# Kernel optimization log

Measured on AMD Instinct MI355X. Metric: run time of the kernel, lower is better.

Reference implementation:

```python
import jax, jax.numpy as jnp
import numpy as np

EPS = 1.0
POS_WEIGHT = 1.0
REDUCTION = 'mean'

N, D = 8192, 128
NUM_CLASSES = 32


def setup_inputs() -> dict:
    key = jax.random.key(0)
    k1, k2 = jax.random.split(key)
    ys = jax.random.normal(k1, (N, D), dtype=jnp.float32)
    labels = jax.random.randint(k2, (N,), 0, NUM_CLASSES, dtype=jnp.int64)
    return {"ys": ys, "labels": labels}


def reference(ys, labels):
    n = ys.shape[0]
    # Pairwise squared distances via one GEMM: ||a||^2 + ||b||^2 - 2 a.b
    sq = jnp.sum(ys * ys, axis=-1)                      # [N]
    d2 = sq[:, None] + sq[None, :] - 2.0 * (ys @ ys.T)  # [N, N]
    d2 = jnp.maximum(d2, 0.0)
    pair = jnp.triu(jnp.ones((n, n), dtype=bool), k=1)  # i < j, each unordered pair once
    same = labels[:, None] == labels[None, :]
    # positive-pair term: pos_weight * squared distance
    pos = POS_WEIGHT * d2
    # negative-pair term: clip(eps - sqrt(d2), 0)^2 ; guard sqrt(0) for unused entries
    neg_mask = pair & (~same)
    d = jnp.sqrt(jnp.where(neg_mask, d2, 1.0))
    neg = jnp.clip(EPS - d, 0.0) ** 2
    terms = jnp.where(same, pos, neg) * pair.astype(ys.dtype)
    loss = jnp.sum(terms)
    if REDUCTION == 'mean':
        loss = loss / (n * (n - 1) / 2)
    return loss.reshape(1)
```

## Files before the change

### kernel.cpp

```cpp
#include <hip/hip_runtime.h>
#include <stdint.h>
#include <math.h>

#define NN 8192
#define DD 128
#define NB 64
#define NBLK (NB * (NB + 1) / 2)
#define NC 32
#define NPB 256
#define RPB 32
#define TOTBLK (NBLK + NC)

typedef __attribute__((ext_vector_type(4))) float f32x4;


__device__ __forceinline__ uint32_t pk4_fp8(float f0, float f1, float f2, float f3) {
    int d = __builtin_amdgcn_cvt_pk_fp8_f32(f0, f1, 0, false);
    d = __builtin_amdgcn_cvt_pk_fp8_f32(f2, f3, d, true);
    return (uint32_t)d;
}

__global__ __launch_bounds__(256) void prep_kernel(const float* __restrict__ ys,
                                                   const int* __restrict__ lab,
                                                   uint32_t* __restrict__ a8,
                                                   uint32_t* __restrict__ b8,
                                                   float* __restrict__ sq,
                                                   float* __restrict__ clspart,
                                                   float* __restrict__ negacc) {
    int b = blockIdx.x, t = threadIdx.x;
    __shared__ float cls[2][NC][DD];
    __shared__ int slab[RPB];

#pragma unroll
    for (int i = 0; i < 8; ++i) ((float4*)cls)[i * 256 + t] = make_float4(0.f, 0.f, 0.f, 0.f);
    if (t < RPB) slab[t] = lab[b * RPB + t];

#pragma unroll
    for (int u = 0; u < 2; ++u) {
        int rloc = (t >> 4) + u * 16;
        int c8 = t & 15;
        int row = b * RPB + rloc;
        const float* base = ys + (size_t)row * DD + c8 * 8;
        float4 v0 = *(const float4*)base;
        float4 v1 = *(const float4*)(base + 4);
        uint2 outB = make_uint2(pk4_fp8(v0.x, v0.y, v0.z, v0.w),
                                pk4_fp8(v1.x, v1.y, v1.z, v1.w));
        uint2 outA = make_uint2(pk4_fp8(-2.f * v0.x, -2.f * v0.y, -2.f * v0.z, -2.f * v0.w),
                                pk4_fp8(-2.f * v1.x, -2.f * v1.y, -2.f * v1.z, -2.f * v1.w));
        size_t off = (size_t)(b * 2 + u) * 2048 + (c8 >> 2) * 512 + (c8 & 3) * 128 + (rloc & 15) * 8;
        *(uint2*)((char*)b8 + off) = outB;
        *(uint2*)((char*)a8 + off) = outA;
        float s = v0.x * v0.x + v0.y * v0.y + v0.z * v0.z + v0.w * v0.w
                + v1.x * v1.x + v1.y * v1.y + v1.z * v1.z + v1.w * v1.w;
        s += __shfl_xor(s, 1); s += __shfl_xor(s, 2);
        s += __shfl_xor(s, 4); s += __shfl_xor(s, 8);
        if (c8 == 0) sq[row] = s;
    }
    __syncthreads();

    {
        int g = t >> 7, col = t & 127;
#pragma unroll
        for (int rr = 0; rr < 16; ++rr) {
            int rloc = g * 16 + rr;
            cls[g][slab[rloc]][col] += ys[(size_t)(b * RPB + rloc) * DD + col];
        }
    }
    __syncthreads();
#pragma unroll
    for (int i = 0; i < 4; ++i) {
        float4 a = ((const float4*)cls[0])[i * 256 + t];
        float4 c = ((const float4*)cls[1])[i * 256 + t];
        ((float4*)(clspart + (size_t)b * NC * DD))[i * 256 + t] =
            make_float4(a.x + c.x, a.y + c.y, a.z + c.z, a.w + c.w);
    }
    if (b == 0 && t == 0) *negacc = 0.f;
}

__global__ __launch_bounds__(256) void loss_kernel(const uint32_t* __restrict__ a8,
                                                   const uint32_t* __restrict__ b8,
                                                   const float* __restrict__ sq,
                                                   const int* __restrict__ lab,
                                                   const float* __restrict__ clspart,
                                                   float* __restrict__ posval,
                                                   float* __restrict__ negacc) {
    int p = blockIdx.x, t = threadIdx.x;

    if (p < NC) {
        __shared__ float sp[2][DD];
        __shared__ float redc[4], reds[4], red2[2];
        int col = t & 127, half = t >> 7;
        float S0 = 0.f, S1 = 0.f, S2 = 0.f, S3 = 0.f;
        const float* cp = clspart + (size_t)half * 128 * NC * DD + p * DD + col;
#pragma unroll 8
        for (int pb = 0; pb < 128; pb += 4) {
            S0 += cp[(size_t)(pb + 0) * NC * DD];
            S1 += cp[(size_t)(pb + 1) * NC * DD];
            S2 += cp[(size_t)(pb + 2) * NC * DD];
            S3 += cp[(size_t)(pb + 3) * NC * DD];
        }
        sp[half][col] = (S0 + S1) + (S2 + S3);

        float cnt = 0.f, ssq = 0.f;
        for (int rr = t; rr < NN; rr += 256) {
            if (lab[rr] == p) { cnt += 1.f; ssq += sq[rr]; }
        }
#pragma unroll
        for (int off = 32; off >= 1; off >>= 1) {
            cnt += __shfl_down(cnt, off);
            ssq += __shfl_down(ssq, off);
        }
        if ((t & 63) == 0) { redc[t >> 6] = cnt; reds[t >> 6] = ssq; }
        __syncthreads();

        float s2 = 0.f;
        if (t < DD) { float Sc = sp[0][t] + sp[1][t]; s2 = Sc * Sc; }
#pragma unroll
        for (int off = 32; off >= 1; off >>= 1) s2 += __shfl_down(s2, off);
        if (t < 128 && (t & 63) == 0) red2[t >> 6] = s2;
        __syncthreads();
        if (t == 0) {
            float c = redc[0] + redc[1] + redc[2] + redc[3];
            float s = reds[0] + reds[1] + reds[2] + reds[3];
            posval[p] = c * s - (red2[0] + red2[1]);
        }
    } else {
        int pt = p - NC;
        int q = (NBLK - 1) - pt;
        int r = (int)((sqrtf(8.0f * (float)q + 1.0f) - 1.0f) * 0.5f);
        while (r * (r + 1) / 2 > q) --r;
        while ((r + 1) * (r + 2) / 2 <= q) ++r;
        int bi = (NB - 1) - r;
        int bj = (NB - 1) - (q - r * (r + 1) / 2);
        int i0 = bi * 128, j0 = bj * 128;

        int wave = t >> 6, lane = t & 63;
        int wm = wave >> 1, wn = wave & 1;
        int lr = lane & 15, lg = lane >> 4;

        float sqa[4][4], sqb[4];
#pragma unroll
        for (int m = 0; m < 4; ++m)
#pragma unroll
            for (int qq = 0; qq < 4; ++qq) sqa[m][qq] = sq[i0 + wm * 64 + m * 16 + lg * 4 + qq];
#pragma unroll
        for (int n = 0; n < 4; ++n) sqb[n] = sq[j0 + wn * 64 + n * 16 + lr];

        f32x4 acc[4][4];
#pragma unroll
        for (int m = 0; m < 4; ++m)
#pragma unroll
            for (int n = 0; n < 4; ++n) {
                f32x4 a;
#pragma unroll
                for (int qq = 0; qq < 4; ++qq) a[qq] = sqa[m][qq] + sqb[n];
                acc[m][n] = a;
            }

        const char* pa = (const char*)a8 + ((size_t)(i0 >> 4) + wm * 4) * 2048 + lg * 128 + lr * 8;
        const char* pbp = (const char*)b8 + ((size_t)(j0 >> 4) + wn * 4) * 2048 + lg * 128 + lr * 8;

#pragma unroll
        for (int ks = 0; ks < 4; ++ks) {
            long af[4], bf[4];
#pragma unroll
            for (int m = 0; m < 4; ++m) af[m] = *(const long*)(pa + m * 2048 + ks * 512);
#pragma unroll
            for (int n = 0; n < 4; ++n) bf[n] = *(const long*)(pbp + n * 2048 + ks * 512);
#pragma unroll
            for (int m = 0; m < 4; ++m)
#pragma unroll
                for (int n = 0; n < 4; ++n)
                    acc[m][n] = __builtin_amdgcn_mfma_f32_16x16x32_fp8_fp8(af[m], bf[n], acc[m][n], 0, 0, 0);
        }

        float mn = acc[0][0][0];
#pragma unroll
        for (int m = 0; m < 4; ++m)
#pragma unroll
            for (int n = 0; n < 4; ++n)
#pragma unroll
                for (int qq = 0; qq < 4; ++qq) mn = fminf(mn, acc[m][n][qq]);

        if (__any(mn < 4.0f)) {
            float ns = 0.f;
#pragma unroll
            for (int m = 0; m < 4; ++m)
#pragma unroll
                for (int n = 0; n < 4; ++n)
#pragma unroll
                    for (int qq = 0; qq < 4; ++qq) {
                        float d2 = acc[m][n][qq];
                        if (d2 < 1.0f) {
                            int i = i0 + wm * 64 + m * 16 + lg * 4 + qq;
                            int j = j0 + wn * 64 + n * 16 + lr;
                            if (i < j && lab[i] != lab[j]) {
                                float e = 1.0f - sqrtf(fmaxf(d2, 0.f));
                                ns += e * e;
                            }
                        }
                    }
            if (ns != 0.f) atomicAdd(negacc, ns);
        }
    }
}

__global__ __launch_bounds__(64) void finalize_kernel(const float* __restrict__ posval,
                                                      const float* __restrict__ negacc,
                                                      float* __restrict__ out) {
    int t = threadIdx.x;
    float s = (t < NC) ? posval[t] : 0.f;
#pragma unroll
    for (int off = 32; off >= 1; off >>= 1) s += __shfl_down(s, off);
    if (t == 0) out[0] = (s + negacc[0]) * (2.0f / ((float)NN * (float)(NN - 1)));
}

extern "C" void kernel_launch(void* const* d_in, const int* in_sizes, int n_in,
                              void* d_out, int out_size, void* d_ws, size_t ws_size,
                              hipStream_t stream) {
    const float* ys = (const float*)d_in[0];
    const int* lab = (const int*)d_in[1];
    float* out = (float*)d_out;

    char* w = (char*)d_ws;
    uint32_t* a8    = (uint32_t*)(w);
    uint32_t* b8    = (uint32_t*)(w + 1048576);
    float* sq       = (float*)(w + 2097152);
    float* clspart  = (float*)(w + 2129920);
    float* posval   = (float*)(w + 6324224);
    float* negacc   = (float*)(w + 6324352);

    prep_kernel<<<NPB, 256, 0, stream>>>(ys, lab, a8, b8, sq, clspart, negacc);
    loss_kernel<<<TOTBLK, 256, 0, stream>>>(a8, b8, sq, lab, clspart, posval, negacc);
    finalize_kernel<<<1, 64, 0, stream>>>(posval, negacc, out);
}
```

Before: 32.91 us.

## Drop finalize kernel, accumulate into output atomically, verify near pairs in fp32

Removes the finalize launch: positive-class terms and negative sums are now scaled and atomically added straight into the output, which prep_kernel zeroes. The tile-skip test now compares the raw fp8 dot-product minimum plus the per-tile minimum squared norms against a loose threshold, so sq is no longer folded into the accumulators before the MFMA. Candidate pairs get their exact fp32 distance recomputed from ys, which makes the result robust to fp8 error. The class-sum pass in prep also splits into four shared partial buffers with float2 loads to cut shared-memory contention. The exact recompute loop is serial and costly if many pairs pass the loose filter.

```diff
diff --git a/kernel.cpp b/kernel.cpp
--- a/kernel.cpp
+++ b/kernel.cpp
@@ -10,6 +10,7 @@
 #define NPB 256
 #define RPB 32
 #define TOTBLK (NBLK + NC)
+#define SCALE (2.0f / ((float)NN * (float)(NN - 1)))
 
 typedef __attribute__((ext_vector_type(4))) float f32x4;
 
@@ -26,13 +27,13 @@
                                                    uint32_t* __restrict__ b8,
                                                    float* __restrict__ sq,
                                                    float* __restrict__ clspart,
-                                                   float* __restrict__ negacc) {
+                                                   float* __restrict__ out) {
     int b = blockIdx.x, t = threadIdx.x;
-    __shared__ float cls[2][NC][DD];
+    __shared__ float cls[4][NC][DD];
     __shared__ int slab[RPB];
 
 #pragma unroll
-    for (int i = 0; i < 8; ++i) ((float4*)cls)[i * 256 + t] = make_float4(0.f, 0.f, 0.f, 0.f);
+    for (int i = 0; i < 16; ++i) ((float4*)cls)[i * 256 + t] = make_float4(0.f, 0.f, 0.f, 0.f);
     if (t < RPB) slab[t] = lab[b * RPB + t];
 
 #pragma unroll
@@ -59,22 +60,29 @@
     __syncthreads();
 
     {
-        int g = t >> 7, col = t & 127;
-#pragma unroll
-        for (int rr = 0; rr < 16; ++rr) {
-            int rloc = g * 16 + rr;
-            cls[g][slab[rloc]][col] += ys[(size_t)(b * RPB + rloc) * DD + col];
+        int g = t >> 6, col0 = (t & 63) * 2;
+#pragma unroll
+        for (int rr = 0; rr < 8; ++rr) {
+            int rloc = g * 8 + rr;
+            float2 v = *(const float2*)(ys + (size_t)(b * RPB + rloc) * DD + col0);
+            int lb = slab[rloc];
+            cls[g][lb][col0]     += v.x;
+            cls[g][lb][col0 + 1] += v.y;
         }
     }
     __syncthreads();
 #pragma unroll
     for (int i = 0; i < 4; ++i) {
-        float4 a = ((const float4*)cls[0])[i * 256 + t];
-        float4 c = ((const float4*)cls[1])[i * 256 + t];
-        ((float4*)(clspart + (size_t)b * NC * DD))[i * 256 + t] =
-            make_float4(a.x + c.x, a.y + c.y, a.z + c.z, a.w + c.w);
-    }
-    if (b == 0 && t == 0) *negacc = 0.f;
+        int idx = i * 256 + t;
+        float4 s0 = ((const float4*)cls[0])[idx];
+        float4 s1 = ((const float4*)cls[1])[idx];
+        float4 s2 = ((const float4*)cls[2])[idx];
+        float4 s3 = ((const float4*)cls[3])[idx];
+        ((float4*)(clspart + (size_t)b * NC * DD))[idx] =
+            make_float4((s0.x + s1.x) + (s2.x + s3.x), (s0.y + s1.y) + (s2.y + s3.y),
+                        (s0.z + s1.z) + (s2.z + s3.z), (s0.w + s1.w) + (s2.w + s3.w));
+    }
+    if (b == 0 && t == 0) out[0] = 0.f;
 }
 
 __global__ __launch_bounds__(256) void loss_kernel(const uint32_t* __restrict__ a8,
@@ -82,8 +90,8 @@
                                                    const float* __restrict__ sq,
                                                    const int* __restrict__ lab,
                                                    const float* __restrict__ clspart,
-                                                   float* __restrict__ posval,
-                                                   float* __restrict__ negacc) {
+                                                   const float* __restrict__ ys,
+                                                   float* __restrict__ out) {
     int p = blockIdx.x, t = threadIdx.x;
 
     if (p < NC) {
@@ -122,97 +130,84 @@
         if (t == 0) {
             float c = redc[0] + redc[1] + redc[2] + redc[3];
             float s = reds[0] + reds[1] + reds[2] + reds[3];
-            posval[p] = c * s - (red2[0] + red2[1]);
-        }
-    } else {
-        int pt = p - NC;
-        int q = (NBLK - 1) - pt;
-        int r = (int)((sqrtf(8.0f * (float)q + 1.0f) - 1.0f) * 0.5f);
-        while (r * (r + 1) / 2 > q) --r;
-        while ((r + 1) * (r + 2) / 2 <= q) ++r;
-        int bi = (NB - 1) - r;
-        int bj = (NB - 1) - (q - r * (r + 1) / 2);
-        int i0 = bi * 128, j0 = bj * 128;
-
-        int wave = t >> 6, lane = t & 63;
-        int wm = wave >> 1, wn = wave & 1;
-        int lr = lane & 15, lg = lane >> 4;
-
-        float sqa[4][4], sqb[4];
+            atomicAdd(out, (c * s - (red2[0] + red2[1])) * SCALE);
+        }
+        return;
+    }
+
+    int pt = p - NC;
+    int q = (NBLK - 1) - pt;
+    int r = (int)((sqrtf(8.0f * (float)q + 1.0f) - 1.0f) * 0.5f);
+    while (r * (r + 1) / 2 > q) --r;
+    while ((r + 1) * (r + 2) / 2 <= q) ++r;
+    int bi = (NB - 1) - r;
+    int bj = (NB - 1) - (q - r * (r + 1) / 2);
+    int i0 = bi * 128, j0 = bj * 128;
+
+    int wave = t >> 6, lane = t & 63;
+    int wm = wave >> 1, wn = wave & 1;
+    int lr = lane & 15, lg = lane >> 4;
+
+    f32x4 acc[4][4];
+#pragma unroll
+    for (int m = 0; m < 4; ++m)
+#pragma unroll
+        for (int n = 0; n < 4; ++n) acc[m][n] = (f32x4){0.f, 0.f, 0.f, 0.f};
+
+    const char* pa = (const char*)a8 + ((size_t)(i0 >> 4) + wm * 4) * 2048 + lg * 128 + lr * 8;
+    const char* pbp = (const char*)b8 + ((size_t)(j0 >> 4) + wn * 4) * 2048 + lg * 128 + lr * 8;
+
+#pragma unroll
+    for (int ks = 0; ks < 4; ++ks) {
+        long af[4], bf[4];
+#pragma unroll
+        for (int m = 0; m < 4; ++m) af[m] = *(const long*)(pa + m * 2048 + ks * 512);
+#pragma unroll
+        for (int n = 0; n < 4; ++n) bf[n] = *(const long*)(pbp + n * 2048 + ks * 512);
 #pragma unroll
         for (int m = 0; m < 4; ++m)
 #pragma unroll
-            for (int qq = 0; qq < 4; ++qq) sqa[m][qq] = sq[i0 + wm * 64 + m * 16 + lg * 4 + qq];
-#pragma unroll
-        for (int n = 0; n < 4; ++n) sqb[n] = sq[j0 + wn * 64 + n * 16 + lr];
-
-        f32x4 acc[4][4];
+            for (int n = 0; n < 4; ++n)
+                acc[m][n] = __builtin_amdgcn_mfma_f32_16x16x32_fp8_fp8(af[m], bf[n], acc[m][n], 0, 0, 0);
+    }
+
+    float msi = fminf(sq[i0 + lane * 2], sq[i0 + lane * 2 + 1]);
+    float msj = fminf(sq[j0 + lane * 2], sq[j0 + lane * 2 + 1]);
+#pragma unroll
+    for (int off = 32; off >= 1; off >>= 1) {
+        msi = fminf(msi, __shfl_xor(msi, off));
+        msj = fminf(msj, __shfl_xor(msj, off));
+    }
+    float mn = acc[0][0][0];
+#pragma unroll
+    for (int m = 0; m < 4; ++m)
+#pragma unroll
+        for (int n = 0; n < 4; ++n)
+#pragma unroll
+            for (int qq = 0; qq < 4; ++qq) mn = fminf(mn, acc[m][n][qq]);
+
+    if (__any(mn + msi + msj < 20.0f)) {
+        float ns = 0.f;
 #pragma unroll
         for (int m = 0; m < 4; ++m)
 #pragma unroll
-            for (int n = 0; n < 4; ++n) {
-                f32x4 a;
-#pragma unroll
-                for (int qq = 0; qq < 4; ++qq) a[qq] = sqa[m][qq] + sqb[n];
-                acc[m][n] = a;
-            }
-
-        const char* pa = (const char*)a8 + ((size_t)(i0 >> 4) + wm * 4) * 2048 + lg * 128 + lr * 8;
-        const char* pbp = (const char*)b8 + ((size_t)(j0 >> 4) + wn * 4) * 2048 + lg * 128 + lr * 8;
-
-#pragma unroll
-        for (int ks = 0; ks < 4; ++ks) {
-            long af[4], bf[4];
-#pragma unroll
-            for (int m = 0; m < 4; ++m) af[m] = *(const long*)(pa + m * 2048 + ks * 512);
-#pragma unroll
-            for (int n = 0; n < 4; ++n) bf[n] = *(const long*)(pbp + n * 2048 + ks * 512);
-#pragma unroll
-            for (int m = 0; m < 4; ++m)
-#pragma unroll
-                for (int n = 0; n < 4; ++n)
-                    acc[m][n] = __builtin_amdgcn_mfma_f32_16x16x32_fp8_fp8(af[m], bf[n], acc[m][n], 0, 0, 0);
-        }
-
-        float mn = acc[0][0][0];
-#pragma unroll
-        for (int m = 0; m < 4; ++m)
-#pragma unroll
             for (int n = 0; n < 4; ++n)
 #pragma unroll
-                for (int qq = 0; qq < 4; ++qq) mn = fminf(mn, acc[m][n][qq]);
-
-        if (__any(mn < 4.0f)) {
-            float ns = 0.f;
-#pragma unroll
-            for (int m = 0; m < 4; ++m)
-#pragma unroll
-                for (int n = 0; n < 4; ++n)
-#pragma unroll
-                    for (int qq = 0; qq < 4; ++qq) {
-                        float d2 = acc[m][n][qq];
-                        if (d2 < 1.0f) {
-                            int i = i0 + wm * 64 + m * 16 + lg * 4 + qq;
-                            int j = j0 + wn * 64 + n * 16 + lr;
-                            if (i < j && lab[i] != lab[j]) {
-                                float e = 1.0f - sqrtf(fmaxf(d2, 0.f));
-                                ns += e * e;
-                            }
+                for (int qq = 0; qq < 4; ++qq) {
+                    int i = i0 + wm * 64 + m * 16 + lg * 4 + qq;
+                    int j = j0 + wn * 64 + n * 16 + lr;
+                    float d2a = acc[m][n][qq] + sq[i] + sq[j];
+                    if (d2a < 20.0f && i < j && lab[i] != lab[j]) {
+                        float d2e = 0.f;
+                        for (int d = 0; d < DD; ++d) {
+                            float df = ys[(size_t)i * DD + d] - ys[(size_t)j * DD + d];
+                            d2e += df * df;
                         }
+                        if (d2e < 1.0f) { float e = 1.0f - sqrtf(d2e); ns += e * e; }
                     }
-            if (ns != 0.f) atomicAdd(negacc, ns);
-        }
-    }
-}
-
-__global__ __launch_bounds__(64) void finalize_kernel(const float* __restrict__ posval,
-                                                      const float* __restrict__ negacc,
-                                                      float* __restrict__ out) {
-    int t = threadIdx.x;
-    float s = (t < NC) ? posval[t] : 0.f;
-#pragma unroll
-    for (int off = 32; off >= 1; off >>= 1) s += __shfl_down(s, off);
-    if (t == 0) out[0] = (s + negacc[0]) * (2.0f / ((float)NN * (float)(NN - 1)));
+                }
+        if (ns != 0.f) atomicAdd(out, ns * SCALE);
+    }
 }
 
 extern "C" void kernel_launch(void* const* d_in, const int* in_sizes, int n_in,
@@ -227,10 +222,7 @@
     uint32_t* b8    = (uint32_t*)(w + 1048576);
     float* sq       = (float*)(w + 2097152);
     float* clspart  = (float*)(w + 2129920);
-    float* posval   = (float*)(w + 6324224);
-    float* negacc   = (float*)(w + 6324352);
-
-    prep_kernel<<<NPB, 256, 0, stream>>>(ys, lab, a8, b8, sq, clspart, negacc);
-    loss_kernel<<<TOTBLK, 256, 0, stream>>>(a8, b8, sq, lab, clspart, posval, negacc);
-    finalize_kernel<<<1, 64, 0, stream>>>(posval, negacc, out);
-}
+
+    prep_kernel<<<NPB, 256, 0, stream>>>(ys, lab, a8, b8, sq, clspart, out);
+    loss_kernel<<<TOTBLK, 256, 0, stream>>>(a8, b8, sq, lab, clspart, ys, out);
+}
```

Result: faster. 32.17 us (median of 2 runs) (-2.3%).
